# Kernel tuning notes

Hardware: AMD Instinct MI355X
Metric: run time of the kernel (lower is better)

## Reference

```python
import jax, jax.numpy as jnp
import numpy as np

# Model dims (match init_kwargs / input_specs)
B, CIN, COUT = 32, 32, 64
H, W = 128, 128
KH, KW = 3, 3
MAXCN = 64                    # max entries in connect_nums_list
HO, WO = H - KH + 1, W - KW + 1   # padding=0, stride=1


def setup_inputs() -> dict:
    key = jax.random.key(0)
    k1, k2, k3, k4 = jax.random.split(key, 4)
    x = jax.random.normal(k1, (B, CIN, H, W), dtype=jnp.float32)
    # padded kernel bank: [out_channel, connection_slot, kh, kw]
    weights = jax.random.normal(k2, (COUT, MAXCN, KH, KW), dtype=jnp.float32)
    # per-pixel bias map per output channel (original inits zeros; random exercises it)
    bias = jax.random.normal(k3, (COUT, HO, WO), dtype=jnp.float32) * 0.1
    connect_nums = jax.random.randint(k4, (COUT,), 1, MAXCN + 1, dtype=jnp.int32)
    return {"x": x, "weights": weights, "bias": bias, "connect_nums": connect_nums}


def reference(x, weights, bias, connect_nums):
    O, J = weights.shape[0], weights.shape[1]
    # mask out kernel slots beyond each channel's connection count
    mask = (jnp.arange(J)[None, :] < connect_nums[:, None]).astype(weights.dtype)  # [O,J]
    # slot j reads input channel j % CIN; conv is linear, so fold duplicate-channel
    # kernels into one effective dense kernel [O, CIN, KH, KW]
    onehot = jax.nn.one_hot(jnp.arange(J) % CIN, CIN, dtype=weights.dtype)  # [J,C]
    kdense = jnp.einsum('ojhw,oj,jc->ochw', weights, mask, onehot)
    out = jax.lax.conv_general_dilated(
        x, kdense, window_strides=(1, 1), padding='VALID',
        dimension_numbers=('NCHW', 'OIHW', 'NCHW'))  # [B,O,HO,WO]
    return out + bias[None]
```

## Files before the change

kernel.cpp:

```cpp
#include <hip/hip_runtime.h>

#define B_    32
#define CIN   32
#define COUT  64
#define H_    128
#define W_    128
#define HO_   126
#define WO_   126
#define MAXCN 64

typedef __attribute__((ext_vector_type(8))) short short8;
typedef __attribute__((ext_vector_type(4))) float floatx4;

static __device__ __forceinline__ unsigned short f2bf(float f) {
    union { float f; unsigned u; } v; v.f = f;
    unsigned r = v.u + 0x7fff + ((v.u >> 16) & 1);
    return (unsigned short)(r >> 16);
}

__global__ void fold_bf16(const float* __restrict__ w,
                          const int* __restrict__ cn,
                          unsigned short* __restrict__ wk) {
    int idx = blockIdx.x * 256 + threadIdx.x;
    if (idx >= 9 * COUT * CIN) return;
    int c   = idx & 31;
    int oc  = (idx >> 5) & 63;
    int tap = idx >> 11;
    int n = cn[oc];
    float v = 0.0f;
    if (c < n)      v += w[(oc * MAXCN + c) * 9 + tap];
    if (c + 32 < n) v += w[(oc * MAXCN + c + 32) * 9 + tap];
    wk[idx] = f2bf(v);
}

__global__ __launch_bounds__(256)
void nchw_to_nhwc_bf16(const float* __restrict__ x,
                       unsigned short* __restrict__ xb) {
    const int b = blockIdx.y, y = blockIdx.x;
    const int t = threadIdx.x;
    const int c8  = t & 3;
    const int xi0 = t >> 2;
    const float* xp = x + (size_t)b * CIN * H_ * W_ + (size_t)y * W_;
#pragma unroll
    for (int it = 0; it < 2; ++it) {
        const int xi = xi0 + it * 64;
        __align__(16) unsigned short v[8];
#pragma unroll
        for (int j = 0; j < 8; ++j) {
            const int c = c8 * 8 + j;
            v[j] = f2bf(xp[(size_t)c * (H_ * W_) + xi]);
        }
        *(uint4*)(xb + (((size_t)b * H_ + y) * W_ + xi) * CIN + c8 * 8) =
            *(const uint4*)v;
    }
}

__global__ __launch_bounds__(256)
void conv_mfma(const unsigned short* __restrict__ xb,
               const unsigned short* __restrict__ wk,
               const float* __restrict__ bias,
               float* __restrict__ out) {
    __shared__ __align__(16) unsigned short xs[18 * 18 * 32];
    __shared__ __align__(16) unsigned short ws[9 * 32 * 32];

    const int tile = blockIdx.x;
    const int ocg  = blockIdx.y;
    const int b    = blockIdx.z;
    const int tx = tile & 7, ty = tile >> 3;
    const int x0 = tx * 16, y0 = ty * 16;
    const int tid = threadIdx.x;

    uint4* xs4 = (uint4*)xs;
    for (int idx = tid; idx < 1296; idx += 256) {
        int yy = idx / 72;
        int r  = idx - yy * 72;
        int xc = r >> 2;
        int cp = r & 3;
        int iy = y0 + yy; if (iy > H_ - 1) iy = H_ - 1;
        int ix = x0 + xc; if (ix > W_ - 1) ix = W_ - 1;
        const uint4* s = (const uint4*)(xb + (((size_t)b * H_ + iy) * W_ + ix) * CIN) + cp;
        xs4[idx] = *s;
    }
    uint4* ws4 = (uint4*)ws;
    const uint4* wk4 = (const uint4*)wk;
    for (int idx = tid; idx < 1152; idx += 256) {
        int tap  = idx >> 7;
        int rem  = idx & 127;
        int oc_l = rem >> 2;
        int cp   = rem & 3;
        ws4[idx] = wk4[tap * 256 + (ocg * 32 + oc_l) * 4 + cp];
    }
    __syncthreads();

    const int w_id = tid >> 6;
    const int lane = tid & 63;
    const int quad = lane >> 4, l16 = lane & 15;

    floatx4 acc[4][2];
#pragma unroll
    for (int i = 0; i < 4; ++i)
#pragma unroll
        for (int t = 0; t < 2; ++t) acc[i][t] = (floatx4)0.0f;

#pragma unroll
    for (int kh = 0; kh < 3; ++kh) {
#pragma unroll
        for (int kw = 0; kw < 3; ++kw) {
            const int tap = kh * 3 + kw;
            short8 a[2], bf[4];
#pragma unroll
            for (int t = 0; t < 2; ++t)
                a[t] = *(const short8*)&ws[((tap * 32 + t * 16 + l16) * 32) + quad * 8];
#pragma unroll
            for (int i = 0; i < 4; ++i)
                bf[i] = *(const short8*)&xs[(((4 * w_id + i + kh) * 18 + l16 + kw) * 32) + quad * 8];
#pragma unroll
            for (int i = 0; i < 4; ++i)
#pragma unroll
                for (int t = 0; t < 2; ++t)
                    acc[i][t] = __builtin_amdgcn_mfma_f32_16x16x32_bf16(a[t], bf[i], acc[i][t], 0, 0, 0);
        }
    }

    const int col = x0 + l16;
#pragma unroll
    for (int i = 0; i < 4; ++i) {
        const int y = y0 + 4 * w_id + i;
        if (y >= HO_ || col >= WO_) continue;
#pragma unroll
        for (int t = 0; t < 2; ++t) {
#pragma unroll
            for (int r = 0; r < 4; ++r) {
                const int oc = ocg * 32 + t * 16 + quad * 4 + r;
                out[(((size_t)b * COUT + oc) * HO_ + y) * WO_ + col] =
                    acc[i][t][r] + bias[((size_t)oc * HO_ + y) * WO_ + col];
            }
        }
    }
}

__global__ void fold_kernel(const float* __restrict__ w,
                            const int* __restrict__ cn,
                            float* __restrict__ kd) {
    int idx = blockIdx.x * blockDim.x + threadIdx.x;
    if (idx >= COUT * CIN * 9) return;
    int t = idx % 9;
    int c = (idx / 9) % CIN;
    int o = idx / (9 * CIN);
    int n = cn[o];
    float v = 0.0f;
    if (c < n)      v += w[(o * MAXCN + c) * 9 + t];
    if (c + 32 < n) v += w[(o * MAXCN + c + 32) * 9 + t];
    kd[idx] = v;
}

__global__ __launch_bounds__(256)
void conv_kernel(const float* __restrict__ x,
                 const float* __restrict__ kd,
                 const float* __restrict__ bias,
                 float* __restrict__ out) {
    __shared__ __align__(16) float xsh[CIN * 18 * 20];
    __shared__ __align__(16) float wsh[16 * 289];
    const int b = blockIdx.z, ocg = blockIdx.y, tile = blockIdx.x;
    const int ty = tile >> 3, txx = tile & 7;
    const int y0 = ty * 16, x0 = txx * 16;
    const int tid = threadIdx.x;
    const float* xbp = x + (size_t)b * CIN * H_ * W_;
    for (int idx = tid; idx < CIN * 18 * 18; idx += 256) {
        int c = idx / 324, rem = idx - c * 324, r = rem / 18, col = rem - r * 18;
        int iy = y0 + r;   if (iy > H_ - 1) iy = H_ - 1;
        int ix = x0 + col; if (ix > W_ - 1) ix = W_ - 1;
        xsh[c * 360 + r * 20 + col] = xbp[(c * H_ + iy) * W_ + ix];
    }
    for (int idx = tid; idx < 16 * 288; idx += 256) {
        int oc = idx / 288, rr = idx - oc * 288;
        wsh[oc * 289 + rr] = kd[(ocg * 16 + oc) * 288 + rr];
    }
    __syncthreads();
    const int oc_l = tid & 15, pb = tid >> 4, pby = pb >> 2, pbx = pb & 3;
    float acc[4][4];
#pragma unroll
    for (int i = 0; i < 4; ++i)
#pragma unroll
        for (int j = 0; j < 4; ++j) acc[i][j] = 0.0f;
    const float* xp = &xsh[(pby * 4) * 20 + pbx * 4];
    const float* wp = &wsh[oc_l * 289];
    for (int c = 0; c < CIN; ++c) {
        float xr[6][6];
#pragma unroll
        for (int r = 0; r < 6; ++r) {
            const float* row = xp + c * 360 + r * 20;
            float4 v4 = *reinterpret_cast<const float4*>(row);
            float2 v2 = *reinterpret_cast<const float2*>(row + 4);
            xr[r][0] = v4.x; xr[r][1] = v4.y; xr[r][2] = v4.z;
            xr[r][3] = v4.w; xr[r][4] = v2.x; xr[r][5] = v2.y;
        }
        float wr[9];
#pragma unroll
        for (int t = 0; t < 9; ++t) wr[t] = wp[c * 9 + t];
#pragma unroll
        for (int kh = 0; kh < 3; ++kh)
#pragma unroll
            for (int kw = 0; kw < 3; ++kw) {
                const float wv = wr[kh * 3 + kw];
#pragma unroll
                for (int i = 0; i < 4; ++i)
#pragma unroll
                    for (int j = 0; j < 4; ++j)
                        acc[i][j] = fmaf(xr[i + kh][j + kw], wv, acc[i][j]);
            }
    }
    const int o = ocg * 16 + oc_l;
    const int yb = y0 + pby * 4, xq0 = x0 + pbx * 4;
    float* ob = out + ((size_t)(b * COUT + o)) * HO_ * WO_;
    const float* bb = bias + (size_t)o * HO_ * WO_;
#pragma unroll
    for (int i = 0; i < 4; ++i) {
        int y = yb + i;
        if (y >= HO_) continue;
#pragma unroll
        for (int j = 0; j < 4; ++j) {
            int xq = xq0 + j;
            if (xq >= WO_) continue;
            ob[y * WO_ + xq] = acc[i][j] + bb[y * WO_ + xq];
        }
    }
}

extern "C" void kernel_launch(void* const* d_in, const int* in_sizes, int n_in,
                              void* d_out, int out_size, void* d_ws, size_t ws_size,
                              hipStream_t stream) {
    const float* x    = (const float*)d_in[0];
    const float* w    = (const float*)d_in[1];
    const float* bias = (const float*)d_in[2];
    const int*   cn   = (const int*)d_in[3];
    float* out = (float*)d_out;

    const size_t XB_BYTES = (size_t)B_ * H_ * W_ * CIN * 2;
    const size_t WK_BYTES = (size_t)9 * COUT * CIN * 2;

    if (ws_size >= XB_BYTES + WK_BYTES) {
        unsigned short* xbuf = (unsigned short*)d_ws;
        unsigned short* wkb  = (unsigned short*)((char*)d_ws + XB_BYTES);
        fold_bf16<<<(9 * COUT * CIN + 255) / 256, 256, 0, stream>>>(w, cn, wkb);
        nchw_to_nhwc_bf16<<<dim3(H_, B_), 256, 0, stream>>>(x, xbuf);
        conv_mfma<<<dim3(64, 2, B_), 256, 0, stream>>>(xbuf, wkb, bias, out);
    } else {
        float* kd = (float*)d_ws;
        fold_kernel<<<(COUT * CIN * 9 + 255) / 256, 256, 0, stream>>>(w, cn, kd);
        dim3 grid(64, 4, B_);
        conv_kernel<<<grid, 256, 0, stream>>>(x, kd, bias, out);
    }
}
```

Baseline: 268.1 us.

## Fuse NCHW-to-bf16 conversion into conv kernel and read weights from global

Removes the separate NCHW-to-NHWC bf16 conversion kernel and its intermediate buffer. The conv kernel now loads the fp32 NCHW input directly and converts to bf16 while filling the shared tile. Weight fragments are read straight from global memory (expected to stay cache-resident) instead of being staged in shared memory, and launch bounds now request higher occupancy. In exchange, the input is reread by both output-channel groups and by overlapping halos, and the fp32 loads are strided across channels.

New measurement: 317.3 us. 18.4% more time.

```diff
diff --git a/kernel.cpp b/kernel.cpp
--- a/kernel.cpp
+++ b/kernel.cpp
@@ -33,35 +33,12 @@
     wk[idx] = f2bf(v);
 }
 
-__global__ __launch_bounds__(256)
-void nchw_to_nhwc_bf16(const float* __restrict__ x,
-                       unsigned short* __restrict__ xb) {
-    const int b = blockIdx.y, y = blockIdx.x;
-    const int t = threadIdx.x;
-    const int c8  = t & 3;
-    const int xi0 = t >> 2;
-    const float* xp = x + (size_t)b * CIN * H_ * W_ + (size_t)y * W_;
-#pragma unroll
-    for (int it = 0; it < 2; ++it) {
-        const int xi = xi0 + it * 64;
-        __align__(16) unsigned short v[8];
-#pragma unroll
-        for (int j = 0; j < 8; ++j) {
-            const int c = c8 * 8 + j;
-            v[j] = f2bf(xp[(size_t)c * (H_ * W_) + xi]);
-        }
-        *(uint4*)(xb + (((size_t)b * H_ + y) * W_ + xi) * CIN + c8 * 8) =
-            *(const uint4*)v;
-    }
-}
-
-__global__ __launch_bounds__(256)
-void conv_mfma(const unsigned short* __restrict__ xb,
-               const unsigned short* __restrict__ wk,
-               const float* __restrict__ bias,
-               float* __restrict__ out) {
+__global__ __launch_bounds__(256, 6)
+void conv_fused(const float* __restrict__ x,
+                const unsigned short* __restrict__ wk,
+                const float* __restrict__ bias,
+                float* __restrict__ out) {
     __shared__ __align__(16) unsigned short xs[18 * 18 * 32];
-    __shared__ __align__(16) unsigned short ws[9 * 32 * 32];
 
     const int tile = blockIdx.x;
     const int ocg  = blockIdx.y;
@@ -70,25 +47,19 @@
     const int x0 = tx * 16, y0 = ty * 16;
     const int tid = threadIdx.x;
 
+    const float* xb = x + (size_t)b * CIN * H_ * W_;
     uint4* xs4 = (uint4*)xs;
     for (int idx = tid; idx < 1296; idx += 256) {
-        int yy = idx / 72;
-        int r  = idx - yy * 72;
-        int xc = r >> 2;
-        int cp = r & 3;
+        int pix = idx >> 2, c8 = idx & 3;
+        int yy = pix / 18, xc = pix - yy * 18;
         int iy = y0 + yy; if (iy > H_ - 1) iy = H_ - 1;
         int ix = x0 + xc; if (ix > W_ - 1) ix = W_ - 1;
-        const uint4* s = (const uint4*)(xb + (((size_t)b * H_ + iy) * W_ + ix) * CIN) + cp;
-        xs4[idx] = *s;
-    }
-    uint4* ws4 = (uint4*)ws;
-    const uint4* wk4 = (const uint4*)wk;
-    for (int idx = tid; idx < 1152; idx += 256) {
-        int tap  = idx >> 7;
-        int rem  = idx & 127;
-        int oc_l = rem >> 2;
-        int cp   = rem & 3;
-        ws4[idx] = wk4[tap * 256 + (ocg * 32 + oc_l) * 4 + cp];
+        const float* s = xb + (size_t)(c8 * 8) * (H_ * W_) + (size_t)iy * W_ + ix;
+        union { unsigned short u16[8]; uint4 u4; } v;
+#pragma unroll
+        for (int j = 0; j < 8; ++j)
+            v.u16[j] = f2bf(s[(size_t)j * (H_ * W_)]);
+        xs4[idx] = v.u4;
     }
     __syncthreads();
 
@@ -110,7 +81,7 @@
             short8 a[2], bf[4];
 #pragma unroll
             for (int t = 0; t < 2; ++t)
-                a[t] = *(const short8*)&ws[((tap * 32 + t * 16 + l16) * 32) + quad * 8];
+                a[t] = *(const short8*)&wk[((size_t)tap * 64 + ocg * 32 + t * 16 + l16) * 32 + quad * 8];
 #pragma unroll
             for (int i = 0; i < 4; ++i)
                 bf[i] = *(const short8*)&xs[(((4 * w_id + i + kh) * 18 + l16 + kw) * 32) + quad * 8];
@@ -236,15 +207,12 @@
     const int*   cn   = (const int*)d_in[3];
     float* out = (float*)d_out;
 
-    const size_t XB_BYTES = (size_t)B_ * H_ * W_ * CIN * 2;
     const size_t WK_BYTES = (size_t)9 * COUT * CIN * 2;
 
-    if (ws_size >= XB_BYTES + WK_BYTES) {
-        unsigned short* xbuf = (unsigned short*)d_ws;
-        unsigned short* wkb  = (unsigned short*)((char*)d_ws + XB_BYTES);
+    if (ws_size >= WK_BYTES) {
+        unsigned short* wkb = (unsigned short*)d_ws;
         fold_bf16<<<(9 * COUT * CIN + 255) / 256, 256, 0, stream>>>(w, cn, wkb);
-        nchw_to_nhwc_bf16<<<dim3(H_, B_), 256, 0, stream>>>(x, xbuf);
-        conv_mfma<<<dim3(64, 2, B_), 256, 0, stream>>>(xbuf, wkb, bias, out);
+        conv_fused<<<dim3(64, 2, B_), 256, 0, stream>>>(x, wkb, bias, out);
     } else {
         float* kd = (float*)d_ws;
         fold_kernel<<<(COUT * CIN * 9 + 255) / 256, 256, 0, stream>>>(w, cn, kd);
```
